# Kernel optimization log

Hardware: AMD Instinct MI355X
Metric: run time of the kernel (lower is better)

## Reference

```python
import jax, jax.numpy as jnp
import numpy as np

NUM_CLASSES = 512
CTX_TYPES = 4
FEAT_DIM = 1024
BATCH = 64
THRESH = 0.5       # context_similarity_threshold
SCALING = 5.0      # scaling_factor
SMOOTH = 0.01      # smoothing_factor


def setup_inputs() -> dict:
    key = jax.random.key(0)
    k1, k2, k3, k4 = jax.random.split(key, 4)
    x = jax.random.normal(k1, (BATCH, NUM_CLASSES, FEAT_DIM), dtype=jnp.float32)
    co_occurrence = jax.random.uniform(k2, (NUM_CLASSES, NUM_CLASSES), dtype=jnp.float32)
    class_counts = jax.random.uniform(k3, (NUM_CLASSES,), dtype=jnp.float32)
    context_embeddings = jax.random.normal(k4, (NUM_CLASSES, CTX_TYPES), dtype=jnp.float32)
    return {"x": x, "co_occurrence": co_occurrence, "class_counts": class_counts,
            "context_embeddings": context_embeddings}


def _build_edge_weights(co, counts, emb):
    C = co.shape[0]
    eye = jnp.eye(C, dtype=co.dtype)
    offdiag = 1.0 - eye
    avg_count = jnp.mean(counts)

    # normalized co-occurrence: (co_ij + s) / sqrt((n_i + s)(n_j + s)), off-diagonal only
    denom = jnp.sqrt((counts[:, None] + SMOOTH) * (counts[None, :] + SMOOTH))
    norm_co = (co + SMOOTH) / denom

    # context affinity: cosine sim * sigmoid(10 * (sim - thr))
    nemb = emb / jnp.linalg.norm(emb, axis=1, keepdims=True)
    sim = nemb @ nemb.T
    affinity = sim * jax.nn.sigmoid((sim - THRESH) * 10.0)

    # class-balance correction
    minc = jnp.minimum(counts[:, None], counts[None, :])
    maxc = jnp.maximum(counts[:, None], counts[None, :])
    balance = jnp.where((minc > SMOOTH) & (maxc > SMOOTH),
                        jnp.log1p(maxc / avg_count) * (minc / maxc),
                        SMOOTH)

    # confidence: 2 / (1 + exp(-co / scale)) - 1
    confidence = 2.0 / (1.0 + jnp.exp(-co / SCALING)) - 1.0

    ew = norm_co * affinity * balance * confidence * offdiag  # zero diagonal as in loops
    ew = jax.nn.softmax(ew * 5.0, axis=1)
    ew = ew * 0.9 + eye * 0.1
    return ew


def reference(x, co_occurrence, class_counts, context_embeddings):
    ew = _build_edge_weights(co_occurrence, class_counts, context_embeddings)
    # bmm with broadcast edge weights: [C,C] @ [B,C,D] -> [B,C,D]
    x_t = jnp.einsum('ij,bjd->bid', ew, x)
    inv_sqrt_d = 1.0 / float(np.sqrt(x.shape[-1]))
    gate = jax.nn.sigmoid(jnp.sum(x * x_t, axis=-1, keepdims=True) * inv_sqrt_d)
    return x * (1.0 - gate) + x_t * gate
```

## Files before the change

### kernel.cpp

```cpp
#include <hip/hip_runtime.h>
#include <hip/hip_bf16.h>
#include <stdint.h>

#define NC 512
#define FD 1024
#define NB 64
#define SMOOTH_ 0.01f
#define STQ 40

typedef __bf16 bf16x8 __attribute__((ext_vector_type(8)));
typedef float f32x4 __attribute__((ext_vector_type(4)));

__device__ __forceinline__ unsigned short f2bf(float f) {
    __hip_bfloat16 h = __float2bfloat16(f);
    return __builtin_bit_cast(unsigned short, h);
}
__device__ __forceinline__ float bf2f(unsigned short u) {
    unsigned int v = (unsigned int)u << 16;
    return __builtin_bit_cast(float, v);
}

__device__ __forceinline__ void gload_lds16(const void* g, void* l) {
    __builtin_amdgcn_global_load_lds(
        (const __attribute__((address_space(1))) void*)(uintptr_t)g,
        (__attribute__((address_space(3))) void*)(uint32_t)(uintptr_t)l,
        16, 0, 0);
}

__global__ __launch_bounds__(256) void build_ew(
    const float* __restrict__ co, const float* __restrict__ counts,
    const float* __restrict__ emb, unsigned short* __restrict__ ew) {
    __shared__ float s_counts[NC];
    __shared__ float s_nemb[NC * 4];
    __shared__ float s_redA[4], s_redM[4], s_redS[4];
    const int i = blockIdx.x;
    const int t = threadIdx.x;
    const int lane = t & 63, wv = t >> 6;

    float c0 = counts[t], c1 = counts[t + 256];
    s_counts[t] = c0;
    s_counts[t + 256] = c1;
    for (int r = t; r < NC; r += 256) {
        float e0 = emb[r * 4 + 0], e1 = emb[r * 4 + 1];
        float e2 = emb[r * 4 + 2], e3 = emb[r * 4 + 3];
        float inv = 1.0f / sqrtf(e0 * e0 + e1 * e1 + e2 * e2 + e3 * e3);
        s_nemb[r * 4 + 0] = e0 * inv;
        s_nemb[r * 4 + 1] = e1 * inv;
        s_nemb[r * 4 + 2] = e2 * inv;
        s_nemb[r * 4 + 3] = e3 * inv;
    }
    float p = c0 + c1;
#pragma unroll
    for (int o = 32; o; o >>= 1) p += __shfl_down(p, o);
    if (lane == 0) s_redA[wv] = p;
    __syncthreads();
    const float avg = (s_redA[0] + s_redA[1] + s_redA[2] + s_redA[3]) * (1.0f / 512.0f);

    const float ci = s_counts[i];
    const float ni0 = s_nemb[i * 4 + 0], ni1 = s_nemb[i * 4 + 1];
    const float ni2 = s_nemb[i * 4 + 2], ni3 = s_nemb[i * 4 + 3];

    float v[2];
#pragma unroll
    for (int u = 0; u < 2; ++u) {
        const int j = t + u * 256;
        const float c = co[i * NC + j];
        const float cj = s_counts[j];
        const float nco = (c + SMOOTH_) / sqrtf((ci + SMOOTH_) * (cj + SMOOTH_));
        const float sim = ni0 * s_nemb[j * 4 + 0] + ni1 * s_nemb[j * 4 + 1] +
                          ni2 * s_nemb[j * 4 + 2] + ni3 * s_nemb[j * 4 + 3];
        const float aff = sim / (1.0f + expf(-(sim - 0.5f) * 10.0f));
        const float mn = fminf(ci, cj), mx = fmaxf(ci, cj);
        const float bal = (mn > SMOOTH_ && mx > SMOOTH_)
                              ? log1pf(mx / avg) * (mn / mx)
                              : SMOOTH_;
        const float conf = 2.0f / (1.0f + expf(-c * 0.2f)) - 1.0f;
        const float e = (j == i) ? 0.0f : nco * aff * bal * conf;
        v[u] = e * 5.0f;
    }
    float m = fmaxf(v[0], v[1]);
#pragma unroll
    for (int o = 32; o; o >>= 1) m = fmaxf(m, __shfl_down(m, o));
    if (lane == 0) s_redM[wv] = m;
    __syncthreads();
    const float rowmax = fmaxf(fmaxf(s_redM[0], s_redM[1]), fmaxf(s_redM[2], s_redM[3]));
    const float e0 = expf(v[0] - rowmax), e1 = expf(v[1] - rowmax);
    float s = e0 + e1;
#pragma unroll
    for (int o = 32; o; o >>= 1) s += __shfl_down(s, o);
    if (lane == 0) s_redS[wv] = s;
    __syncthreads();
    const float scale = 0.9f / (s_redS[0] + s_redS[1] + s_redS[2] + s_redS[3]);
    const float w0 = e0 * scale + ((t == i) ? 0.1f : 0.0f);
    const float w1 = e1 * scale + ((t + 256 == i) ? 0.1f : 0.0f);
    ew[i * NC + t] = f2bf(w0);
    ew[i * NC + t + 256] = f2bf(w1);
}

__global__ __launch_bounds__(256) void gemm_tr2(
    const unsigned short* __restrict__ ew, const float* __restrict__ x,
    unsigned short* __restrict__ xt) {
    __shared__ __align__(16) unsigned short smA[2][128 * 32];
    __shared__ __align__(16) unsigned short smT[2][128 * STQ];
    const int t = threadIdx.x;
    const int lane = t & 63, w = t >> 6;
    const int wr = w >> 1, wc = w & 1;

    const int bid = blockIdx.x;
    const int slot = bid & 7, idx = bid >> 3;
    const int bq = idx >> 5, inner = idx & 31;
    const int b = slot + bq * 8;
    const int i_t = inner >> 3, d_t = inner & 7;
    const int i0 = i_t * 128, d0 = d_t * 128;

    const unsigned short* gA = ew + (size_t)(i0 + (t >> 2)) * NC + (t & 3) * 8;

    const int jp = t >> 4, m = t & 15;
    const float* gB0 = x + ((size_t)(b * NC) + 2 * jp) * FD + d0 + m;
    const float* gB1 = gB0 + FD;

    const int lr = lane & 15, kidx = lane >> 4;

    f32x4 acc[4][4];
#pragma unroll
    for (int mi = 0; mi < 4; ++mi)
#pragma unroll
        for (int ni = 0; ni < 4; ++ni) acc[mi][ni] = (f32x4){0.f, 0.f, 0.f, 0.f};

    float r0[8], r1[8];

    auto LOAD_B = [&](int s) {
        const size_t off = (size_t)s * 32 * FD;
#pragma unroll
        for (int e = 0; e < 8; ++e) {
            r0[e] = gB0[off + 16 * e];
            r1[e] = gB1[off + 16 * e];
        }
    };
    auto STAGE_A = [&](int s, int pb) {
        const int k0 = s * 32;
        gload_lds16(gA + k0, &smA[pb][t * 8]);
        gload_lds16(gA + (size_t)64 * NC + k0, &smA[pb][64 * 32 + t * 8]);
    };
    auto STAGE_B = [&](int pb) {
        unsigned int* bt32 = reinterpret_cast<unsigned int*>(smT[pb]);
#pragma unroll
        for (int e = 0; e < 8; ++e) {
            const int d = m + 16 * e;
            const unsigned int val =
                (unsigned int)f2bf(r0[e]) | ((unsigned int)f2bf(r1[e]) << 16);
            bt32[d * (STQ / 2) + jp] = val;
        }
    };

    LOAD_B(0);
    STAGE_A(0, 0);
    STAGE_B(0);
    LOAD_B(1);

    int p = 0;
    for (int s = 0; s < 16; ++s) {
        __syncthreads();
        if (s < 15) {
            STAGE_A(s + 1, p ^ 1);
            STAGE_B(p ^ 1);
        }
        if (s < 14) LOAD_B(s + 2);

        const bf16x8* A8 = reinterpret_cast<const bf16x8*>(smA[p]);
        bf16x8 aF[4];
#pragma unroll
        for (int mi = 0; mi < 4; ++mi)
            aF[mi] = A8[(wr * 64 + mi * 16 + lr) * 4 + kidx];
        bf16x8 bF[4];
#pragma unroll
        for (int ni = 0; ni < 4; ++ni) {
            const int nb = wc * 64 + ni * 16 + lr;
            bF[ni] = *reinterpret_cast<const bf16x8*>(&smT[p][nb * STQ + kidx * 8]);
        }
#pragma unroll
        for (int mi = 0; mi < 4; ++mi)
#pragma unroll
            for (int ni = 0; ni < 4; ++ni)
                acc[mi][ni] = __builtin_amdgcn_mfma_f32_16x16x32_bf16(
                    aF[mi], bF[ni], acc[mi][ni], 0, 0, 0);
        p ^= 1;
    }

    const int r0e = (lane >> 4) * 4;
#pragma unroll
    for (int mi = 0; mi < 4; ++mi)
#pragma unroll
        for (int ni = 0; ni < 4; ++ni)
#pragma unroll
            for (int r = 0; r < 4; ++r) {
                const size_t R = (size_t)(b * NC + i0 + wr * 64 + mi * 16 + r0e + r);
                xt[R * FD + d0 + wc * 64 + ni * 16 + lr] = f2bf(acc[mi][ni][r]);
            }
}

__global__ __launch_bounds__(256) void gate_out(
    const float* __restrict__ x, const unsigned short* __restrict__ xt,
    float* __restrict__ out) {
    __shared__ float s[4];
    const int row = blockIdx.x;
    const int t = threadIdx.x;
    const size_t base = (size_t)row * FD + t * 4;
    const float4 xv = *reinterpret_cast<const float4*>(x + base);
    const ushort4 uv = *reinterpret_cast<const ushort4*>(xt + base);
    const float t0 = bf2f(uv.x), t1 = bf2f(uv.y), t2 = bf2f(uv.z), t3 = bf2f(uv.w);
    float p = xv.x * t0 + xv.y * t1 + xv.z * t2 + xv.w * t3;
#pragma unroll
    for (int o = 32; o; o >>= 1) p += __shfl_down(p, o);
    if ((t & 63) == 0) s[t >> 6] = p;
    __syncthreads();
    const float dot = s[0] + s[1] + s[2] + s[3];
    const float g = 1.0f / (1.0f + expf(-dot * 0.03125f));
    float4 ov;
    ov.x = xv.x * (1.0f - g) + t0 * g;
    ov.y = xv.y * (1.0f - g) + t1 * g;
    ov.z = xv.z * (1.0f - g) + t2 * g;
    ov.w = xv.w * (1.0f - g) + t3 * g;
    *reinterpret_cast<float4*>(out + base) = ov;
}

extern "C" void kernel_launch(void* const* d_in, const int* in_sizes, int n_in,
                              void* d_out, int out_size, void* d_ws, size_t ws_size,
                              hipStream_t stream) {
    const float* x = (const float*)d_in[0];
    const float* co = (const float*)d_in[1];
    const float* counts = (const float*)d_in[2];
    const float* emb = (const float*)d_in[3];
    float* out = (float*)d_out;

    unsigned short* ew = (unsigned short*)d_ws;
    unsigned short* xt = (unsigned short*)((char*)d_ws + (1u << 20));

    build_ew<<<NC, 256, 0, stream>>>(co, counts, emb, ew);
    gemm_tr2<<<2048, 256, 0, stream>>>(ew, x, xt);
    gate_out<<<NB * NC, 256, 0, stream>>>(x, xt, out);
}
```

Before: 121.8 us.

## Load GEMM A operand directly into registers instead of via LDS

The edge-weight (A) operand of the batched GEMM is now loaded straight from global memory into MFMA fragment registers, which removes the LDS staging buffer for A and its global_load_lds path. The per-iteration __syncthreads is replaced by an explicit lgkmcnt wait plus s_barrier placed after the MFMAs, with the next A tile loaded at that point. Launch bounds request 3 blocks per CU. The trade-off is less LDS traffic and a lighter barrier against global A loads that are redundant across the two column-waves and less coalesced, and that may stall the MFMAs because the s_waitcnt only covers LDS traffic, not the vector memory loads.

```diff
diff --git a/kernel.cpp b/kernel.cpp
--- a/kernel.cpp
+++ b/kernel.cpp
@@ -18,13 +18,6 @@
 __device__ __forceinline__ float bf2f(unsigned short u) {
     unsigned int v = (unsigned int)u << 16;
     return __builtin_bit_cast(float, v);
-}
-
-__device__ __forceinline__ void gload_lds16(const void* g, void* l) {
-    __builtin_amdgcn_global_load_lds(
-        (const __attribute__((address_space(1))) void*)(uintptr_t)g,
-        (__attribute__((address_space(3))) void*)(uint32_t)(uintptr_t)l,
-        16, 0, 0);
 }
 
 __global__ __launch_bounds__(256) void build_ew(
@@ -97,10 +90,9 @@
     ew[i * NC + t + 256] = f2bf(w1);
 }
 
-__global__ __launch_bounds__(256) void gemm_tr2(
+__global__ __launch_bounds__(256, 3) void gemm_areg(
     const unsigned short* __restrict__ ew, const float* __restrict__ x,
     unsigned short* __restrict__ xt) {
-    __shared__ __align__(16) unsigned short smA[2][128 * 32];
     __shared__ __align__(16) unsigned short smT[2][128 * STQ];
     const int t = threadIdx.x;
     const int lane = t & 63, w = t >> 6;
@@ -113,22 +105,32 @@
     const int i_t = inner >> 3, d_t = inner & 7;
     const int i0 = i_t * 128, d0 = d_t * 128;
 
-    const unsigned short* gA = ew + (size_t)(i0 + (t >> 2)) * NC + (t & 3) * 8;
+    const int lr = lane & 15, kidx = lane >> 4;
+
+    const unsigned short* ewp[4];
+#pragma unroll
+    for (int mi = 0; mi < 4; ++mi)
+        ewp[mi] = ew + (size_t)(i0 + wr * 64 + mi * 16 + lr) * NC + kidx * 8;
 
     const int jp = t >> 4, m = t & 15;
     const float* gB0 = x + ((size_t)(b * NC) + 2 * jp) * FD + d0 + m;
     const float* gB1 = gB0 + FD;
 
-    const int lr = lane & 15, kidx = lane >> 4;
-
     f32x4 acc[4][4];
 #pragma unroll
     for (int mi = 0; mi < 4; ++mi)
 #pragma unroll
         for (int ni = 0; ni < 4; ++ni) acc[mi][ni] = (f32x4){0.f, 0.f, 0.f, 0.f};
 
+    bf16x8 aF[4];
     float r0[8], r1[8];
 
+    auto LOAD_A = [&](int s) {
+        const int off = s * 32;
+#pragma unroll
+        for (int mi = 0; mi < 4; ++mi)
+            aF[mi] = *reinterpret_cast<const bf16x8*>(ewp[mi] + off);
+    };
     auto LOAD_B = [&](int s) {
         const size_t off = (size_t)s * 32 * FD;
 #pragma unroll
@@ -136,11 +138,6 @@
             r0[e] = gB0[off + 16 * e];
             r1[e] = gB1[off + 16 * e];
         }
-    };
-    auto STAGE_A = [&](int s, int pb) {
-        const int k0 = s * 32;
-        gload_lds16(gA + k0, &smA[pb][t * 8]);
-        gload_lds16(gA + (size_t)64 * NC + k0, &smA[pb][64 * 32 + t * 8]);
     };
     auto STAGE_B = [&](int pb) {
         unsigned int* bt32 = reinterpret_cast<unsigned int*>(smT[pb]);
@@ -153,25 +150,19 @@
         }
     };
 
+    LOAD_A(0);
     LOAD_B(0);
-    STAGE_A(0, 0);
     STAGE_B(0);
     LOAD_B(1);
+    asm volatile("s_waitcnt lgkmcnt(0)" ::: "memory");
+    __builtin_amdgcn_sched_barrier(0);
+    __builtin_amdgcn_s_barrier();
 
     int p = 0;
     for (int s = 0; s < 16; ++s) {
-        __syncthreads();
-        if (s < 15) {
-            STAGE_A(s + 1, p ^ 1);
-            STAGE_B(p ^ 1);
-        }
+        if (s < 15) STAGE_B(p ^ 1);
         if (s < 14) LOAD_B(s + 2);
 
-        const bf16x8* A8 = reinterpret_cast<const bf16x8*>(smA[p]);
-        bf16x8 aF[4];
-#pragma unroll
-        for (int mi = 0; mi < 4; ++mi)
-            aF[mi] = A8[(wr * 64 + mi * 16 + lr) * 4 + kidx];
         bf16x8 bF[4];
 #pragma unroll
         for (int ni = 0; ni < 4; ++ni) {
@@ -184,6 +175,13 @@
             for (int ni = 0; ni < 4; ++ni)
                 acc[mi][ni] = __builtin_amdgcn_mfma_f32_16x16x32_bf16(
                     aF[mi], bF[ni], acc[mi][ni], 0, 0, 0);
+
+        if (s < 15) {
+            LOAD_A(s + 1);
+            asm volatile("s_waitcnt lgkmcnt(0)" ::: "memory");
+            __builtin_amdgcn_sched_barrier(0);
+            __builtin_amdgcn_s_barrier();
+        }
         p ^= 1;
     }
 
@@ -237,6 +235,6 @@
     unsigned short* xt = (unsigned short*)((char*)d_ws + (1u << 20));
 
     build_ew<<<NC, 256, 0, stream>>>(co, counts, emb, ew);
-    gemm_tr2<<<2048, 256, 0, stream>>>(ew, x, xt);
+    gemm_areg<<<2048, 256, 0, stream>>>(ew, x, xt);
     gate_out<<<NB * NC, 256, 0, stream>>>(x, xt, out);
 }
```

Result: slower. 147.5 us (+21.1%).
